# Kernel optimization log

Hardware: AMD Instinct MI355X
Metric: run time of the kernel (lower is better)

## Reference

```python
import jax, jax.numpy as jnp
import numpy as np
from jax import lax

B, T, C, H, N = 4, 1024, 2048, 32, 64
KVH = 8            # kv heads -> kv_dim = 512, n_rep = 4
GN_EPS = 0.00064   # group_norm eps from Step3


def _l2norm(x):
    # torch F.normalize(p=2, dim=-1) with eps=1e-12
    n = jnp.linalg.norm(x, axis=-1, keepdims=True)
    return x / jnp.maximum(n, 1e-12)


def _rwkv7_scan(r, decay, k, v, aa, bb, state):
    # all inputs (B,T,H,N); state (B,H,N,N) with layout [value, key]
    def step(S, inp):
        r_t, d_t, k_t, v_t, a_t, b_t = inp  # each (B,H,N)
        sa = jnp.einsum('bhik,bhk->bhi', S, a_t)
        S = (S * d_t[:, :, None, :]
             + sa[..., None] * b_t[:, :, None, :]
             + v_t[..., None] * k_t[:, :, None, :])
        y = jnp.einsum('bhik,bhk->bhi', S, r_t)
        return S, y
    xs = tuple(jnp.moveaxis(t, 1, 0) for t in (r, decay, k, v, aa, bb))  # (T,B,H,N)
    state, ys = lax.scan(step, state, xs)
    return jnp.moveaxis(ys, 0, 1), state  # (B,T,H,N), (B,H,N,N)


def _forward(x, v_first, state, R, R_bias, K, K_bias, V, V_bias, O, O_bias,
             w0, w1, w2, a0, a1, a2, v0, v1, v2, k_k, k_a, r_k, ln_w, ln_b):
    # ---- Step1: projections + gates (hybrid_matmul -> plain matmul in fp32 ref) ----
    r = x @ R.T + R_bias                                   # (B,T,C)
    w_raw = -jax.nn.softplus(-(w0 + jnp.tanh(x @ w1) @ w2)) - 0.6
    k = x @ K.T + K_bias                                   # (B,T,512)
    v = x @ V.T + V_bias
    n_rep = C // K.shape[0]
    k = jnp.repeat(k.reshape(B, T, KVH, N), n_rep, axis=2).reshape(B, T, C)
    v = jnp.repeat(v.reshape(B, T, KVH, N), n_rep, axis=2).reshape(B, T, C)
    a = jax.nn.sigmoid(a0 + (x @ a1) @ a2)
    kk = _l2norm((k * k_k).reshape(B, T, H, N)).reshape(B, T, C)
    k = k * (1.0 + (a - 1.0) * k_a)
    # layer_id != 0: cross-layer value blending
    v = v + (v_first - v) * jax.nn.sigmoid(v0 + (x @ v1) @ v2)
    aa = -kk
    bb = kk * a
    # ---- Step2: fused recurrent rwkv7 (fp32 state) ----
    decay = jnp.exp(-jnp.exp(w_raw.astype(jnp.float32)))
    rs = lambda t: t.astype(jnp.float32).reshape(B, T, H, N)
    y, state_out = _rwkv7_scan(rs(r), decay.reshape(B, T, H, N), rs(k), rs(v), rs(aa), rs(bb), state)
    # ---- Step3: group norm over (T, N) per (batch, head) as in the (B,C,T) permute ----
    mean = y.mean(axis=(1, 3), keepdims=True)
    var = ((y - mean) ** 2).mean(axis=(1, 3), keepdims=True)
    yn = (y - mean) * lax.rsqrt(var + GN_EPS)
    xx = (yn * ln_w.reshape(H, N) + ln_b.reshape(H, N)).reshape(B, T, C)
    bonus = ((r.reshape(B, T, H, N) * k.reshape(B, T, H, N) * r_k.reshape(H, N))
             .sum(-1, keepdims=True) * v.reshape(B, T, H, N)).reshape(B, T, C)
    xx = xx + bonus
    out = xx @ O.T + O_bias
    return out


def setup_inputs() -> dict:
    key = jax.random.key(0)
    ks = jax.random.split(key, 25)
    g = lambda i, shape, s: jax.random.normal(ks[i], shape, dtype=jnp.float32) * s
    return {
        'x': g(0, (B, T, C), 1.0),
        'v_first': g(1, (B, T, C), 1.0),
        'state': jnp.zeros((B, H, N, N), dtype=jnp.float32),
        'R': g(2, (C, C), 0.02), 'R_bias': jnp.zeros((C,), jnp.float32),
        'K': g(3, (KVH * N, C), 0.02), 'K_bias': jnp.zeros((KVH * N,), jnp.float32),
        'V': g(4, (KVH * N, C), 0.02), 'V_bias': jnp.zeros((KVH * N,), jnp.float32),
        'O': g(5, (C, C), 0.02), 'O_bias': jnp.zeros((C,), jnp.float32),
        'w0': g(6, (C,), 0.1), 'w1': g(7, (C, 64), 0.05), 'w2': g(8, (64, C), 0.05),
        'a0': g(9, (C,), 0.1), 'a1': g(10, (C, 64), 0.05), 'a2': g(11, (64, C), 0.05),
        'v0': g(12, (C,), 0.1), 'v1': g(13, (C, 32), 0.05), 'v2': g(14, (32, C), 0.05),
        'k_k': 1.0 + g(15, (C,), 0.05),
        'k_a': 1.0 + g(16, (C,), 0.05),
        'r_k': g(17, (C,), 0.1),
        'ln_w': jnp.ones((C,), jnp.float32),
        'ln_b': jnp.zeros((C,), jnp.float32),
    }


def reference(x, v_first, state, R, R_bias, K, K_bias, V, V_bias, O, O_bias,
              w0, w1, w2, a0, a1, a2, v0, v1, v2, k_k, k_a, r_k, ln_w, ln_b):
    return _forward(x, v_first, state, R, R_bias, K, K_bias, V, V_bias, O, O_bias,
                    w0, w1, w2, a0, a1, a2, v0, v1, v2, k_k, k_a, r_k, ln_w, ln_b)
```

## Files before the change

kernel.cpp:

```cpp
#include <hip/hip_runtime.h>
#include <hip/hip_bf16.h>
#include <math.h>

typedef __attribute__((ext_vector_type(8))) short bf16x8;
typedef __attribute__((ext_vector_type(4))) float f32x4;

__device__ __forceinline__ unsigned short f2b(float f) {
  unsigned u = __float_as_uint(f);
  unsigned r = (u + 0x7FFF + ((u >> 16) & 1)) >> 16;
  return (unsigned short)r;
}

__device__ __forceinline__ void async16(const void* g, void* l) {
  __builtin_amdgcn_global_load_lds(
      (const __attribute__((address_space(1))) unsigned int*)(g),
      (__attribute__((address_space(3))) unsigned int*)(l), 16, 0, 0);
}

__device__ __forceinline__ void async4(const void* g, void* l) {
  __builtin_amdgcn_global_load_lds(
      (const __attribute__((address_space(1))) unsigned int*)(g),
      (__attribute__((address_space(3))) unsigned int*)(l), 4, 0, 0);
}

__device__ __forceinline__ float rowsum16(float x) {
  x += __int_as_float(__builtin_amdgcn_update_dpp(0, __float_as_int(x), 0x121, 0xF, 0xF, false));
  x += __int_as_float(__builtin_amdgcn_update_dpp(0, __float_as_int(x), 0x122, 0xF, 0xF, false));
  x += __int_as_float(__builtin_amdgcn_update_dpp(0, __float_as_int(x), 0x124, 0xF, 0xF, false));
  x += __int_as_float(__builtin_amdgcn_update_dpp(0, __float_as_int(x), 0x128, 0xF, 0xF, false));
  return x;
}

__global__ __launch_bounds__(256) void cvt4_kernel(
    const float* __restrict__ x, const float* __restrict__ R,
    const float* __restrict__ K, const float* __restrict__ V,
    unsigned short* __restrict__ xb, unsigned short* __restrict__ RKVb)
{
  const int bid = blockIdx.x;
  const float* s; unsigned short* d; int i;
  if (bid < 8192)       { s = x; d = xb; i = bid * 256 + threadIdx.x; }
  else if (bid < 12288) { s = R; d = RKVb; i = (bid - 8192) * 256 + threadIdx.x; }
  else if (bid < 13312) { s = K; d = RKVb + 2048 * 2048; i = (bid - 12288) * 256 + threadIdx.x; }
  else                  { s = V; d = RKVb + 2560 * 2048; i = (bid - 13312) * 256 + threadIdx.x; }
  float4 v = ((const float4*)s)[i];
  ushort4 o;
  o.x = f2b(v.x); o.y = f2b(v.y); o.z = f2b(v.z); o.w = f2b(v.w);
  ((ushort4*)d)[i] = o;
}

__global__ __launch_bounds__(256) void cvt_bf16(
    const float* __restrict__ s, unsigned short* __restrict__ d, int n4)
{
  int i = blockIdx.x * 256 + threadIdx.x;
  if (i < n4) {
    float4 v = ((const float4*)s)[i];
    ushort4 o;
    o.x = f2b(v.x); o.y = f2b(v.y); o.z = f2b(v.z); o.w = f2b(v.w);
    ((ushort4*)d)[i] = o;
  }
}

__global__ __launch_bounds__(256) void tcvt_all(
    const float* __restrict__ w1, const float* __restrict__ a1,
    const float* __restrict__ v1, const float* __restrict__ w2,
    const float* __restrict__ a2, const float* __restrict__ v2,
    unsigned short* __restrict__ Bcat, unsigned short* __restrict__ w2t,
    unsigned short* __restrict__ a2t, unsigned short* __restrict__ v2t)
{
  const int r = blockIdx.x >> 5, i = blockIdx.x & 31;
  const float* in; unsigned short* out; int Kd, Nd, ors, bx, by;
  switch (r) {
    case 0:  in = w1; out = Bcat;             Kd = 2048; Nd = 64;   ors = 2048; bx = 0; by = i; break;
    case 1:  in = a1; out = Bcat + 64 * 2048; Kd = 2048; Nd = 64;   ors = 2048; bx = 0; by = i; break;
    case 2:  in = v1; out = Bcat + 128 * 2048; Kd = 2048; Nd = 32;  ors = 2048; bx = 0; by = i; break;
    case 3:  in = w2; out = w2t;              Kd = 64;   Nd = 2048; ors = 64;   bx = i; by = 0; break;
    case 4:  in = a2; out = a2t;              Kd = 64;   Nd = 2048; ors = 64;   bx = i; by = 0; break;
    default: in = v2; out = v2t;              Kd = 32;   Nd = 2048; ors = 32;   bx = i; by = 0; break;
  }
  __shared__ unsigned short tile[64][65];
  const int tx = threadIdx.x & 63, ty = threadIdx.x >> 6;
  const int n0 = bx * 64, k0 = by * 64;
  #pragma unroll
  for (int j = 0; j < 16; ++j) {
    const int k = k0 + j * 4 + ty;
    const int n = n0 + tx;
    unsigned short v = 0;
    if (k < Kd && n < Nd) v = f2b(in[(size_t)k * Nd + n]);
    tile[j * 4 + ty][tx] = v;
  }
  __syncthreads();
  #pragma unroll
  for (int j = 0; j < 16; ++j) {
    const int n = n0 + j * 4 + ty;
    const int k = k0 + tx;
    if (n < Nd && k < Kd) out[(size_t)n * ors + k] = tile[tx][j * 4 + ty];
  }
}

template<int OUTBF16, int ACT>
__global__ __launch_bounds__(256) void gemm_mfma(
    const unsigned short* __restrict__ A, int lda,
    const unsigned short* __restrict__ B, int ldb,
    const float* __restrict__ bias, void* __restrict__ Cv, int ldc,
    int M, int N, int K)
{
  __shared__ __align__(16) unsigned short As[128 * 32];
  __shared__ __align__(16) unsigned short Bs[128 * 32];
  const int tid = threadIdx.x;
  const int w = tid >> 6, lane = tid & 63;
  const int wr = (w >> 1) * 64, wc = (w & 1) * 64;
  const int row0 = blockIdx.y * 128, col0 = blockIdx.x * 128;

  f32x4 acc[4][4];
  #pragma unroll
  for (int i = 0; i < 4; ++i)
    #pragma unroll
    for (int j = 0; j < 4; ++j)
      acc[i][j] = (f32x4){0.f, 0.f, 0.f, 0.f};

  const int srow = w * 32 + (lane >> 2);
  const int scol = (lane & 3) * 8;
  const int brow0 = (col0 + srow < N) ? (col0 + srow) : 0;
  const int brow1 = (col0 + srow + 16 < N) ? (col0 + srow + 16) : 0;
  const unsigned short* gA0 = A + (size_t)(row0 + srow) * lda + scol;
  const unsigned short* gA1 = gA0 + (size_t)16 * lda;
  const unsigned short* gB0 = B + (size_t)brow0 * ldb + scol;
  const unsigned short* gB1 = B + (size_t)brow1 * ldb + scol;
  unsigned short* lA0 = As + w * 1024;
  unsigned short* lA1 = As + w * 1024 + 512;
  unsigned short* lB0 = Bs + w * 1024;
  unsigned short* lB1 = Bs + w * 1024 + 512;

  const int m16 = lane & 15;
  const int q8  = (lane >> 4) * 8;

  for (int k0 = 0; k0 < K; k0 += 32) {
    async16(gA0, lA0);
    async16(gA1, lA1);
    async16(gB0, lB0);
    async16(gB1, lB1);
    gA0 += 32; gA1 += 32; gB0 += 32; gB1 += 32;
    __syncthreads();
    bf16x8 af[4], bfr[4];
    #pragma unroll
    for (int i = 0; i < 4; ++i) {
      af[i]  = *(const bf16x8*)(As + (wr + i * 16 + m16) * 32 + q8);
      bfr[i] = *(const bf16x8*)(Bs + (wc + i * 16 + m16) * 32 + q8);
    }
    #pragma unroll
    for (int i = 0; i < 4; ++i)
      #pragma unroll
      for (int j = 0; j < 4; ++j)
        acc[i][j] = __builtin_amdgcn_mfma_f32_16x16x32_bf16(af[i], bfr[j], acc[i][j], 0, 0, 0);
    __syncthreads();
  }

  #pragma unroll
  for (int j = 0; j < 4; ++j) {
    const int c_ = col0 + wc + j * 16 + (lane & 15);
    if (c_ < N) {
      const float bv = bias ? bias[c_] : 0.f;
      #pragma unroll
      for (int i = 0; i < 4; ++i) {
        const int r_ = row0 + wr + i * 16 + (lane >> 4) * 4;
        #pragma unroll
        for (int t4 = 0; t4 < 4; ++t4) {
          float v = acc[i][j][t4] + bv;
          if (ACT == 2 && c_ < 64) v = tanhf(v);
          if (OUTBF16)
            ((unsigned short*)Cv)[(size_t)(r_ + t4) * ldc + c_] = f2b(v);
          else
            ((float*)Cv)[(size_t)(r_ + t4) * ldc + c_] = v;
        }
      }
    }
  }
}

__global__ __launch_bounds__(256) void gemm_rkv(
    const unsigned short* __restrict__ A, const unsigned short* __restrict__ B,
    const float* __restrict__ Rb_, const float* __restrict__ Kb_,
    const float* __restrict__ Vb_,
    float* __restrict__ Cr, float* __restrict__ Ck, float* __restrict__ Cvv)
{
  __shared__ __align__(16) unsigned short As[128 * 32];
  __shared__ __align__(16) unsigned short Bs[128 * 32];
  const int tid = threadIdx.x;
  const int w = tid >> 6, lane = tid & 63;
  const int wr = (w >> 1) * 64, wc = (w & 1) * 64;
  const int row0 = blockIdx.y * 128, col0 = blockIdx.x * 128;

  float* Cd; int ldc, cbase; const float* bias;
  if (col0 < 2048)      { Cd = Cr;  ldc = 2048; cbase = col0;        bias = Rb_; }
  else if (col0 < 2560) { Cd = Ck;  ldc = 512;  cbase = col0 - 2048; bias = Kb_; }
  else                  { Cd = Cvv; ldc = 512;  cbase = col0 - 2560; bias = Vb_; }

  f32x4 acc[4][4];
  #pragma unroll
  for (int i = 0; i < 4; ++i)
    #pragma unroll
    for (int j = 0; j < 4; ++j)
      acc[i][j] = (f32x4){0.f, 0.f, 0.f, 0.f};

  const int srow = w * 32 + (lane >> 2);
  const int scol = (lane & 3) * 8;
  const unsigned short* gA0 = A + (size_t)(row0 + srow) * 2048 + scol;
  const unsigned short* gA1 = gA0 + (size_t)16 * 2048;
  const unsigned short* gB0 = B + (size_t)(col0 + srow) * 2048 + scol;
  const unsigned short* gB1 = gB0 + (size_t)16 * 2048;
  unsigned short* lA0 = As + w * 1024;
  unsigned short* lA1 = As + w * 1024 + 512;
  unsigned short* lB0 = Bs + w * 1024;
  unsigned short* lB1 = Bs + w * 1024 + 512;

  const int m16 = lane & 15;
  const int q8  = (lane >> 4) * 8;

  for (int k0 = 0; k0 < 2048; k0 += 32) {
    async16(gA0, lA0);
    async16(gA1, lA1);
    async16(gB0, lB0);
    async16(gB1, lB1);
    gA0 += 32; gA1 += 32; gB0 += 32; gB1 += 32;
    __syncthreads();
    bf16x8 af[4], bfr[4];
    #pragma unroll
    for (int i = 0; i < 4; ++i) {
      af[i]  = *(const bf16x8*)(As + (wr + i * 16 + m16) * 32 + q8);
      bfr[i] = *(const bf16x8*)(Bs + (wc + i * 16 + m16) * 32 + q8);
    }
    #pragma unroll
    for (int i = 0; i < 4; ++i)
      #pragma unroll
      for (int j = 0; j < 4; ++j)
        acc[i][j] = __builtin_amdgcn_mfma_f32_16x16x32_bf16(af[i], bfr[j], acc[i][j], 0, 0, 0);
    __syncthreads();
  }

  #pragma unroll
  for (int j = 0; j < 4; ++j) {
    const int c_ = cbase + wc + j * 16 + (lane & 15);
    const float bv = bias[c_];
    #pragma unroll
    for (int i = 0; i < 4; ++i) {
      const int r_ = row0 + wr + i * 16 + (lane >> 4) * 4;
      #pragma unroll
      for (int t4 = 0; t4 < 4; ++t4)
        Cd[(size_t)(r_ + t4) * ldc + c_] = acc[i][j][t4] + bv;
    }
  }
}

__global__ __launch_bounds__(256) void prep_kernel(
    const float* __restrict__ k_buf, const float* __restrict__ v_buf,
    float* wt_decay, const float* __restrict__ at, float* vt_vf,
    const float* __restrict__ v_first,
    const float* __restrict__ w0, const float* __restrict__ a0,
    const float* __restrict__ v0, const float* __restrict__ k_k,
    const float* __restrict__ k_a,
    float* __restrict__ kf, float* __restrict__ aaq, float* __restrict__ bbq)
{
  const int row = blockIdx.x;
  const int tid = threadIdx.x;
  const int c0 = tid << 3;
  const int h = tid >> 3;
  const int kvoff = (h >> 2) << 6;
  const size_t base = (size_t)row * 2048;
  const size_t kvrow = (size_t)row * 512;
  float kr[8], kkr[8];
  float ss = 0.f;
  #pragma unroll
  for (int e = 0; e < 8; ++e) {
    const int c = c0 + e;
    const float kv = k_buf[kvrow + kvoff + (c & 63)];
    kr[e] = kv;
    const float t = kv * k_k[c];
    kkr[e] = t;
    ss = fmaf(t, t, ss);
  }
  ss += __shfl_xor(ss, 1);
  ss += __shfl_xor(ss, 2);
  ss += __shfl_xor(ss, 4);
  const float inv = 1.f / fmaxf(sqrtf(ss), 1e-12f);
  #pragma unroll
  for (int e = 0; e < 8; ++e) {
    const int c = c0 + e;
    const size_t idx = base + c;
    const float kk = kkr[e] * inv;
    const float a = 1.f / (1.f + expf(-(a0[c] + at[idx])));
    const float u = w0[c] + wt_decay[idx];
    const float sig_u = 1.f / (1.f + expf(-u));
    wt_decay[idx] = expf(-0.5488116360940264f * sig_u);
    kf[idx] = kr[e] * fmaf(a - 1.f, k_a[c], 1.f);
    const float vr = v_buf[kvrow + kvoff + (c & 63)];
    const float sv = 1.f / (1.f + expf(-(v0[c] + vt_vf[idx])));
    vt_vf[idx] = vr + (v_first[idx] - vr) * sv;
    aaq[idx] = -kk;
    bbq[idx] = kk * a;
  }
}

#define WB(n) asm volatile("s_waitcnt vmcnt(" #n ") lgkmcnt(0)\n\ts_barrier" ::: "memory")
#define BAR2() asm volatile("s_waitcnt lgkmcnt(0)\n\ts_barrier" ::: "memory")

__global__ __launch_bounds__(256) void scan_kernel(
    const float* __restrict__ rB, const float* __restrict__ dB,
    const float* __restrict__ kB, const float* __restrict__ vB,
    const float* __restrict__ aB, const float* __restrict__ bB,
    const float* __restrict__ state, float* __restrict__ y,
    float* __restrict__ part)
{
  __shared__ float lds[11776];
  const int tid = threadIdx.x;
  const int bid = blockIdx.x;
  const int xcd = bid & 7, j = bid >> 3;
  const int half = j & 1, bhq = j >> 1;
  const int bh = (bhq << 3) | xcd;
  const int widx = tid >> 6;
  const int lane = tid & 63;
  const int rg = lane >> 4;
  const int colg = lane & 15;
  const int r0b = (widx << 3) + (rg << 1);
  const int r0 = (half << 5) + r0b;
  const int b = bh >> 5, h = bh & 31;

  float4 S0 = *(const float4*)(state + (size_t)bh * 4096 + r0 * 64 + (colg << 2));
  float4 S1 = *(const float4*)(state + (size_t)bh * 4096 + (r0 + 1) * 64 + (colg << 2));

  const unsigned cb = (unsigned)((b * 1024) * 2048 + h * 64);
  const unsigned gcol = (unsigned)(colg << 2);
  const unsigned ldsseg = (unsigned)(widx << 8);
  const unsigned vrow = (unsigned)(half << 5);

  float sacc = 0.f, ssacc = 0.f;

  #define STAGE(step0, bofs) do {                                            \
    const unsigned go_ = cb + (unsigned)((step0) + (tid >> 4)) * 2048u;      \
    async16(rB + go_ + gcol, lds + (bofs) + 0 * 1024 + ldsseg);              \
    async16(dB + go_ + gcol, lds + (bofs) + 1 * 1024 + ldsseg);              \
    async16(kB + go_ + gcol, lds + (bofs) + 2 * 1024 + ldsseg);              \
    async16(aB + go_ + gcol, lds + (bofs) + 3 * 1024 + ldsseg);              \
    async16(bB + go_ + gcol, lds + (bofs) + 4 * 1024 + ldsseg);              \
    const unsigned gv0_ = cb + (unsigned)((step0) + (tid >> 5)) * 2048u      \
                          + vrow + (unsigned)(tid & 31);                     \
    async4(vB + gv0_, lds + (bofs) + 5120 + (widx << 6));                    \
    const unsigned t2_ = (unsigned)tid + 256u;                               \
    const unsigned gv1_ = cb + (unsigned)((step0) + (t2_ >> 5)) * 2048u      \
                          + vrow + (unsigned)(t2_ & 31);                     \
    async4(vB + gv1_, lds + (bofs) + 5120 + 256 + (widx << 6));              \
  } while (0)

  #define PROCESS(bofs) do {                                                 \
    const int orr_ = (bofs) + 0 * 1024 + (colg << 2);                        \
    const int od_  = (bofs) + 1 * 1024 + (colg << 2);                        \
    const int ok_  = (bofs) + 2 * 1024 + (colg << 2);                        \
    const int oa_  = (bofs) + 3 * 1024 + (colg << 2);                        \
    const int ob_  = (bofs) + 4 * 1024 + (colg << 2);                        \
    const int ov_  = (bofs) + 5120 + r0b;                                    \
    _Pragma("unroll")                                                        \
    for (int s = 0; s < 16; ++s) {                                           \
      const float4 av = *(const float4*)(lds + oa_ + s * 64);                \
      const float4 dv = *(const float4*)(lds + od_ + s * 64);                \
      const float4 bv = *(const float4*)(lds + ob_ + s * 64);                \
      const float4 kv = *(const float4*)(lds + ok_ + s * 64);                \
      const float4 rv = *(const float4*)(lds + orr_ + s * 64);               \
      const float2 vv = *(const float2*)(lds + ov_ + (s << 5));              \
      float t0a = fmaf(S0.y, av.y, S0.x * av.x);                             \
      t0a = fmaf(S0.z, av.z, t0a);                                           \
      t0a = fmaf(S0.w, av.w, t0a);                                           \
      float t0b = fmaf(S1.y, av.y, S1.x * av.x);                             \
      t0b = fmaf(S1.z, av.z, t0b);                                           \
      t0b = fmaf(S1.w, av.w, t0b);                                           \
      const float sa0 = rowsum16(t0a);                                       \
      const float sa1 = rowsum16(t0b);                                       \
      S0.x = fmaf(S0.x, dv.x, fmaf(sa0, bv.x, vv.x * kv.x));                 \
      S0.y = fmaf(S0.y, dv.y, fmaf(sa0, bv.y, vv.x * kv.y));                 \
      S0.z = fmaf(S0.z, dv.z, fmaf(sa0, bv.z, vv.x * kv.z));                 \
      S0.w = fmaf(S0.w, dv.w, fmaf(sa0, bv.w, vv.x * kv.w));                 \
      S1.x = fmaf(S1.x, dv.x, fmaf(sa1, bv.x, vv.y * kv.x));                 \
      S1.y = fmaf(S1.y, dv.y, fmaf(sa1, bv.y, vv.y * kv.y));                 \
      S1.z = fmaf(S1.z, dv.z, fmaf(sa1, bv.z, vv.y * kv.z));                 \
      S1.w = fmaf(S1.w, dv.w, fmaf(sa1, bv.w, vv.y * kv.w));                 \
      float t1a = fmaf(S0.y, rv.y, S0.x * rv.x);                             \
      t1a = fmaf(S0.z, rv.z, t1a);                                           \
      t1a = fmaf(S0.w, rv.w, t1a);                                           \
      float t1b = fmaf(S1.y, rv.y, S1.x * rv.x);                             \
      t1b = fmaf(S1.z, rv.z, t1b);                                           \
      t1b = fmaf(S1.w, rv.w, t1b);                                           \
      const float y0 = rowsum16(t1a);                                        \
      const float y1 = rowsum16(t1b);                                        \
      if (colg == 0) {                                                       \
        *(float2*)(lds + 11264 + (s << 5) + r0b) = make_float2(y0, y1);      \
        sacc += y0 + y1;                                                     \
        ssacc = fmaf(y0, y0, fmaf(y1, y1, ssacc));                           \
      }                                                                      \
    }                                                                        \
  } while (0)

  #define YSTORE(step0) do {                                                 \
    const float2 v_ = *(const float2*)(lds + 11264 + ((tid >> 4) << 5)       \
                                       + ((tid & 15) << 1));                 \
    *(float2*)(y + cb + (unsigned)((step0) + (tid >> 4)) * 2048u             \
               + vrow + (unsigned)((tid & 15) << 1)) = v_;                   \
  } while (0)

  STAGE(0, 0);
  STAGE(16, 5632);

  WB(7);
  PROCESS(0);
  BAR2();
  YSTORE(0);
  STAGE(32, 0);

  for (int c = 1; c <= 62; ++c) {
    const int bofs = (c & 1) ? 5632 : 0;
    WB(8);
    PROCESS(bofs);
    BAR2();
    YSTORE(c << 4);
    if (c < 62) STAGE((c + 2) << 4, bofs);
  }

  WB(1);
  PROCESS(5632);
  BAR2();
  YSTORE(1008);

  sacc  += __shfl_xor(sacc, 16);
  sacc  += __shfl_xor(sacc, 32);
  ssacc += __shfl_xor(ssacc, 16);
  ssacc += __shfl_xor(ssacc, 32);
  __syncthreads();
  if (lane == 0) { lds[widx] = sacc; lds[4 + widx] = ssacc; }
  __syncthreads();
  if (tid == 0) {
    const float s_  = lds[0] + lds[1] + lds[2] + lds[3];
    const float ss_ = lds[4] + lds[5] + lds[6] + lds[7];
    ((float2*)part)[(bh << 1) + half] = make_float2(s_, ss_);
  }

  #undef STAGE
  #undef PROCESS
  #undef YSTORE
}

__global__ __launch_bounds__(256) void gapply_kernel(
    const float* __restrict__ y, const float* __restrict__ rB,
    const float* __restrict__ kf, const float* __restrict__ vf,
    const float* __restrict__ part, const float* __restrict__ r_k,
    const float* __restrict__ ln_w, const float* __restrict__ ln_b,
    unsigned short* __restrict__ xxb)
{
  const int row = blockIdx.x;
  const int b = row >> 10;
  const int tid = threadIdx.x;
  const int h = tid >> 3;
  const int bh = b * 32 + h;
  float s = 0.f, ss = 0.f;
  #pragma unroll
  for (int j = 0; j < 2; ++j) {
    const float2 pr = ((const float2*)part)[(bh << 1) + j];
    s += pr.x; ss += pr.y;
  }
  const float mean = s * (1.f / 65536.f);
  const float rstd = rsqrtf(ss * (1.f / 65536.f) - mean * mean + 0.00064f);
  const int c0 = tid << 3;
  const size_t base = (size_t)row * 2048 + c0;
  float yv[8], vv[8];
  float p = 0.f;
  #pragma unroll
  for (int e = 0; e < 8; ++e) {
    yv[e] = y[base + e];
    vv[e] = vf[base + e];
    p = fmaf(rB[base + e] * kf[base + e], r_k[c0 + e], p);
  }
  p += __shfl_xor(p, 1);
  p += __shfl_xor(p, 2);
  p += __shfl_xor(p, 4);
  #pragma unroll
  for (int e = 0; e < 8; ++e) {
    const float yn = (yv[e] - mean) * rstd;
    xxb[base + e] = f2b(fmaf(yn, ln_w[c0 + e], ln_b[c0 + e]) + p * vv[e]);
  }
}

extern "C" void kernel_launch(void* const* d_in, const int* in_sizes, int n_in,
                              void* d_out, int out_size, void* d_ws, size_t ws_size,
                              hipStream_t stream) {
  const float* x       = (const float*)d_in[0];
  const float* v_first = (const float*)d_in[1];
  const float* state   = (const float*)d_in[2];
  const float* Rw      = (const float*)d_in[3];
  const float* R_bias  = (const float*)d_in[4];
  const float* Kw      = (const float*)d_in[5];
  const float* K_bias  = (const float*)d_in[6];
  const float* Vw      = (const float*)d_in[7];
  const float* V_bias  = (const float*)d_in[8];
  const float* Ow      = (const float*)d_in[9];
  const float* O_bias  = (const float*)d_in[10];
  const float* w0      = (const float*)d_in[11];
  const float* w1      = (const float*)d_in[12];
  const float* w2      = (const float*)d_in[13];
  const float* a0      = (const float*)d_in[14];
  const float* a1      = (const float*)d_in[15];
  const float* a2      = (const float*)d_in[16];
  const float* v0      = (const float*)d_in[17];
  const float* v1      = (const float*)d_in[18];
  const float* v2      = (const float*)d_in[19];
  const float* k_k     = (const float*)d_in[20];
  const float* k_a     = (const float*)d_in[21];
  const float* r_k     = (const float*)d_in[22];
  const float* ln_w    = (const float*)d_in[23];
  const float* ln_b    = (const float*)d_in[24];

  float* ws = (float*)d_ws;
  float* r_buf = ws;
  float* k_buf = r_buf + 8388608;
  float* v_buf = k_buf + 2097152;
  float* wt    = v_buf + 2097152;
  float* at    = wt    + 8388608;
  float* vt    = at    + 8388608;
  float* kf    = vt    + 8388608;
  float* aaq   = kf    + 8388608;
  float* bbq   = aaq   + 8388608;
  float* part  = bbq   + 8388608;
  unsigned short* xb   = (unsigned short*)bbq;
  unsigned short* RKVb = (unsigned short*)kf;
  unsigned short* hcat = (unsigned short*)(kf + 3200000);
  unsigned short* Bcat = (unsigned short*)(kf + 3600000);
  unsigned short* w2t  = (unsigned short*)(kf + 3800000);
  unsigned short* a2t  = (unsigned short*)(kf + 3900000);
  unsigned short* v2t  = (unsigned short*)(kf + 4000000);
  unsigned short* Ob   = (unsigned short*)wt;
  unsigned short* xxb  = (unsigned short*)aaq;

  dim3 blk(256);
  cvt4_kernel<<<14336, blk, 0, stream>>>(x, Rw, Kw, Vw, xb, RKVb);
  tcvt_all<<<192, blk, 0, stream>>>(w1, a1, v1, w2, a2, v2, Bcat, w2t, a2t, v2t);
  gemm_mfma<1,2><<<dim3(2, 32), blk, 0, stream>>>(xb, 2048, Bcat, 2048, nullptr,
                                                  hcat, 160, 4096, 160, 2048);
  gemm_rkv<<<dim3(24, 32), blk, 0, stream>>>(xb, RKVb, R_bias, K_bias, V_bias,
                                             r_buf, k_buf, v_buf);
  gemm_mfma<0,0><<<dim3(16, 32), blk, 0, stream>>>(hcat, 160, w2t, 64, nullptr,
                                                   wt, 2048, 4096, 2048, 64);
  gemm_mfma<0,0><<<dim3(16, 32), blk, 0, stream>>>(hcat + 64, 160, a2t, 64, nullptr,
                                                   at, 2048, 4096, 2048, 64);
  gemm_mfma<0,0><<<dim3(16, 32), blk, 0, stream>>>(hcat + 128, 160, v2t, 32, nullptr,
                                                   vt, 2048, 4096, 2048, 32);
  prep_kernel<<<4096, blk, 0, stream>>>(k_buf, v_buf, wt, at, vt, v_first,
                                        w0, a0, v0, k_k, k_a, kf, aaq, bbq);
  float* ybuf = at;
  scan_kernel<<<256, blk, 0, stream>>>(r_buf, wt, kf, vt, aaq, bbq, state, ybuf,
                                       part);
  cvt_bf16<<<4096, blk, 0, stream>>>(Ow, Ob, 1048576);
  gapply_kernel<<<4096, blk, 0, stream>>>(ybuf, r_buf, kf, vt, part, r_k,
                                          ln_w, ln_b, xxb);
  gemm_mfma<0,0><<<dim3(16, 32), blk, 0, stream>>>(xxb, 2048, Ob, 2048, O_bias,
                                                   (float*)d_out, 2048, 4096, 2048, 2048);
}
```

Before: 823.2 us.

## Pack r/k and a/b as bf16 pairs and split scan over 4 row blocks

```diff
diff --git a/kernel.cpp b/kernel.cpp
--- a/kernel.cpp
+++ b/kernel.cpp
@@ -15,12 +15,6 @@
   __builtin_amdgcn_global_load_lds(
       (const __attribute__((address_space(1))) unsigned int*)(g),
       (__attribute__((address_space(3))) unsigned int*)(l), 16, 0, 0);
-}
-
-__device__ __forceinline__ void async4(const void* g, void* l) {
-  __builtin_amdgcn_global_load_lds(
-      (const __attribute__((address_space(1))) unsigned int*)(g),
-      (__attribute__((address_space(3))) unsigned int*)(l), 4, 0, 0);
 }
 
 __device__ __forceinline__ float rowsum16(float x) {
@@ -253,12 +247,13 @@
 
 __global__ __launch_bounds__(256) void prep_kernel(
     const float* __restrict__ k_buf, const float* __restrict__ v_buf,
+    const float* __restrict__ r_buf,
     float* wt_decay, const float* __restrict__ at, float* vt_vf,
     const float* __restrict__ v_first,
     const float* __restrict__ w0, const float* __restrict__ a0,
     const float* __restrict__ v0, const float* __restrict__ k_k,
     const float* __restrict__ k_a,
-    float* __restrict__ kf, float* __restrict__ aaq, float* __restrict__ bbq)
+    unsigned* __restrict__ rk_pk, unsigned* __restrict__ ab_pk)
 {
   const int row = blockIdx.x;
   const int tid = threadIdx.x;
@@ -291,12 +286,12 @@
     const float u = w0[c] + wt_decay[idx];
     const float sig_u = 1.f / (1.f + expf(-u));
     wt_decay[idx] = expf(-0.5488116360940264f * sig_u);
-    kf[idx] = kr[e] * fmaf(a - 1.f, k_a[c], 1.f);
+    const float kfin = kr[e] * fmaf(a - 1.f, k_a[c], 1.f);
     const float vr = v_buf[kvrow + kvoff + (c & 63)];
     const float sv = 1.f / (1.f + expf(-(v0[c] + vt_vf[idx])));
     vt_vf[idx] = vr + (v_first[idx] - vr) * sv;
-    aaq[idx] = -kk;
-    bbq[idx] = kk * a;
+    rk_pk[idx] = ((unsigned)f2b(kfin) << 16) | (unsigned)f2b(r_buf[idx]);
+    ab_pk[idx] = ((unsigned)f2b(-kk) << 16) | (unsigned)f2b(kk * a);
   }
 }
 
@@ -304,128 +299,119 @@
 #define BAR2() asm volatile("s_waitcnt lgkmcnt(0)\n\ts_barrier" ::: "memory")
 
 __global__ __launch_bounds__(256) void scan_kernel(
-    const float* __restrict__ rB, const float* __restrict__ dB,
-    const float* __restrict__ kB, const float* __restrict__ vB,
-    const float* __restrict__ aB, const float* __restrict__ bB,
+    const unsigned* __restrict__ rkB, const unsigned* __restrict__ abB,
+    const float* __restrict__ dB, const float* __restrict__ vB,
     const float* __restrict__ state, float* __restrict__ y,
     float* __restrict__ part)
 {
-  __shared__ float lds[11776];
+  __shared__ float lds[6912];
+  unsigned* ldsU = (unsigned*)lds;
   const int tid = threadIdx.x;
   const int bid = blockIdx.x;
-  const int xcd = bid & 7, j = bid >> 3;
-  const int half = j & 1, bhq = j >> 1;
-  const int bh = (bhq << 3) | xcd;
+  const int xcd = bid & 7, bj = bid >> 3;
+  const int m = bj & 3, gq = bj >> 2;
+  const int bh = (gq << 3) | xcd;
   const int widx = tid >> 6;
   const int lane = tid & 63;
   const int rg = lane >> 4;
   const int colg = lane & 15;
-  const int r0b = (widx << 3) + (rg << 1);
-  const int r0 = (half << 5) + r0b;
+  const int rowb = (widx << 2) + rg;
+  const int row = (m << 4) + rowb;
   const int b = bh >> 5, h = bh & 31;
 
-  float4 S0 = *(const float4*)(state + (size_t)bh * 4096 + r0 * 64 + (colg << 2));
-  float4 S1 = *(const float4*)(state + (size_t)bh * 4096 + (r0 + 1) * 64 + (colg << 2));
+  float4 S = *(const float4*)(state + (size_t)bh * 4096 + row * 64 + (colg << 2));
 
   const unsigned cb = (unsigned)((b * 1024) * 2048 + h * 64);
-  const unsigned gcol = (unsigned)(colg << 2);
-  const unsigned ldsseg = (unsigned)(widx << 8);
-  const unsigned vrow = (unsigned)(half << 5);
+  const unsigned sstep = (unsigned)(tid >> 4);
+  const unsigned scol = (unsigned)((tid & 15) << 2);
+  const unsigned lseg = (unsigned)(widx << 8);
 
   float sacc = 0.f, ssacc = 0.f;
 
   #define STAGE(step0, bofs) do {                                            \
-    const unsigned go_ = cb + (unsigned)((step0) + (tid >> 4)) * 2048u;      \
-    async16(rB + go_ + gcol, lds + (bofs) + 0 * 1024 + ldsseg);              \
-    async16(dB + go_ + gcol, lds + (bofs) + 1 * 1024 + ldsseg);              \
-    async16(kB + go_ + gcol, lds + (bofs) + 2 * 1024 + ldsseg);              \
-    async16(aB + go_ + gcol, lds + (bofs) + 3 * 1024 + ldsseg);              \
-    async16(bB + go_ + gcol, lds + (bofs) + 4 * 1024 + ldsseg);              \
-    const unsigned gv0_ = cb + (unsigned)((step0) + (tid >> 5)) * 2048u      \
-                          + vrow + (unsigned)(tid & 31);                     \
-    async4(vB + gv0_, lds + (bofs) + 5120 + (widx << 6));                    \
-    const unsigned t2_ = (unsigned)tid + 256u;                               \
-    const unsigned gv1_ = cb + (unsigned)((step0) + (t2_ >> 5)) * 2048u      \
-                          + vrow + (unsigned)(t2_ & 31);                     \
-    async4(vB + gv1_, lds + (bofs) + 5120 + 256 + (widx << 6));              \
+    const unsigned go_ = cb + ((step0) + sstep) * 2048u + scol;              \
+    async16(rkB + go_, ldsU + (bofs) + lseg);                                \
+    async16(abB + go_, ldsU + (bofs) + 1024 + lseg);                         \
+    async16(dB + go_,  lds + (bofs) + 2048 + lseg);                          \
+    if (lane < 16) {                                                         \
+      const unsigned gv_ = cb + ((step0) + (unsigned)(widx << 2)             \
+                                 + (unsigned)(lane >> 2)) * 2048u            \
+                           + (unsigned)(m << 4) + (unsigned)((lane & 3) << 2); \
+      async16(vB + gv_, lds + (bofs) + 3072 + (widx << 6));                  \
+    }                                                                        \
   } while (0)
 
   #define PROCESS(bofs) do {                                                 \
-    const int orr_ = (bofs) + 0 * 1024 + (colg << 2);                        \
-    const int od_  = (bofs) + 1 * 1024 + (colg << 2);                        \
-    const int ok_  = (bofs) + 2 * 1024 + (colg << 2);                        \
-    const int oa_  = (bofs) + 3 * 1024 + (colg << 2);                        \
-    const int ob_  = (bofs) + 4 * 1024 + (colg << 2);                        \
-    const int ov_  = (bofs) + 5120 + r0b;                                    \
     _Pragma("unroll")                                                        \
     for (int s = 0; s < 16; ++s) {                                           \
-      const float4 av = *(const float4*)(lds + oa_ + s * 64);                \
-      const float4 dv = *(const float4*)(lds + od_ + s * 64);                \
-      const float4 bv = *(const float4*)(lds + ob_ + s * 64);                \
-      const float4 kv = *(const float4*)(lds + ok_ + s * 64);                \
-      const float4 rv = *(const float4*)(lds + orr_ + s * 64);               \
-      const float2 vv = *(const float2*)(lds + ov_ + (s << 5));              \
-      float t0a = fmaf(S0.y, av.y, S0.x * av.x);                             \
-      t0a = fmaf(S0.z, av.z, t0a);                                           \
-      t0a = fmaf(S0.w, av.w, t0a);                                           \
-      float t0b = fmaf(S1.y, av.y, S1.x * av.x);                             \
-      t0b = fmaf(S1.z, av.z, t0b);                                           \
-      t0b = fmaf(S1.w, av.w, t0b);                                           \
-      const float sa0 = rowsum16(t0a);                                       \
-      const float sa1 = rowsum16(t0b);                                       \
-      S0.x = fmaf(S0.x, dv.x, fmaf(sa0, bv.x, vv.x * kv.x));                 \
-      S0.y = fmaf(S0.y, dv.y, fmaf(sa0, bv.y, vv.x * kv.y));                 \
-      S0.z = fmaf(S0.z, dv.z, fmaf(sa0, bv.z, vv.x * kv.z));                 \
-      S0.w = fmaf(S0.w, dv.w, fmaf(sa0, bv.w, vv.x * kv.w));                 \
-      S1.x = fmaf(S1.x, dv.x, fmaf(sa1, bv.x, vv.y * kv.x));                 \
-      S1.y = fmaf(S1.y, dv.y, fmaf(sa1, bv.y, vv.y * kv.y));                 \
-      S1.z = fmaf(S1.z, dv.z, fmaf(sa1, bv.z, vv.y * kv.z));                 \
-      S1.w = fmaf(S1.w, dv.w, fmaf(sa1, bv.w, vv.y * kv.w));                 \
-      float t1a = fmaf(S0.y, rv.y, S0.x * rv.x);                             \
-      t1a = fmaf(S0.z, rv.z, t1a);                                           \
-      t1a = fmaf(S0.w, rv.w, t1a);                                           \
-      float t1b = fmaf(S1.y, rv.y, S1.x * rv.x);                             \
-      t1b = fmaf(S1.z, rv.z, t1b);                                           \
-      t1b = fmaf(S1.w, rv.w, t1b);                                           \
-      const float y0 = rowsum16(t1a);                                        \
-      const float y1 = rowsum16(t1b);                                        \
+      const uint4 rkw = *(const uint4*)(ldsU + (bofs) + s * 64 + (colg << 2)); \
+      const uint4 abw = *(const uint4*)(ldsU + (bofs) + 1024 + s * 64 + (colg << 2)); \
+      const float4 dv = *(const float4*)(lds + (bofs) + 2048 + s * 64 + (colg << 2)); \
+      const float vv = lds[(bofs) + 3072 + (s << 4) + rowb];                 \
+      const float aa0 = __uint_as_float(abw.x & 0xffff0000u);                \
+      const float aa1 = __uint_as_float(abw.y & 0xffff0000u);                \
+      const float aa2 = __uint_as_float(abw.z & 0xffff0000u);                \
+      const float aa3 = __uint_as_float(abw.w & 0xffff0000u);                \
+      const float bb0 = __uint_as_float(abw.x << 16);                        \
+      const float bb1 = __uint_as_float(abw.y << 16);                        \
+      const float bb2 = __uint_as_float(abw.z << 16);                        \
+      const float bb3 = __uint_as_float(abw.w << 16);                        \
+      const float k0 = __uint_as_float(rkw.x & 0xffff0000u);                 \
+      const float k1 = __uint_as_float(rkw.y & 0xffff0000u);                 \
+      const float k2 = __uint_as_float(rkw.z & 0xffff0000u);                 \
+      const float k3 = __uint_as_float(rkw.w & 0xffff0000u);                 \
+      const float r0 = __uint_as_float(rkw.x << 16);                         \
+      const float r1 = __uint_as_float(rkw.y << 16);                         \
+      const float r2 = __uint_as_float(rkw.z << 16);                         \
+      const float r3 = __uint_as_float(rkw.w << 16);                         \
+      float t0 = fmaf(S.y, aa1, S.x * aa0);                                  \
+      t0 = fmaf(S.z, aa2, t0);                                               \
+      t0 = fmaf(S.w, aa3, t0);                                               \
+      const float sa = rowsum16(t0);                                         \
+      S.x = fmaf(S.x, dv.x, fmaf(sa, bb0, vv * k0));                         \
+      S.y = fmaf(S.y, dv.y, fmaf(sa, bb1, vv * k1));                         \
+      S.z = fmaf(S.z, dv.z, fmaf(sa, bb2, vv * k2));                         \
+      S.w = fmaf(S.w, dv.w, fmaf(sa, bb3, vv * k3));                         \
+      float t1 = fmaf(S.y, r1, S.x * r0);                                    \
+      t1 = fmaf(S.z, r2, t1);                                                \
+      t1 = fmaf(S.w, r3, t1);                                                \
+      const float yv = rowsum16(t1);                                         \
       if (colg == 0) {                                                       \
-        *(float2*)(lds + 11264 + (s << 5) + r0b) = make_float2(y0, y1);      \
-        sacc += y0 + y1;                                                     \
-        ssacc = fmaf(y0, y0, fmaf(y1, y1, ssacc));                           \
+        lds[6656 + (s << 4) + rowb] = yv;                                    \
+        sacc += yv;                                                          \
+        ssacc = fmaf(yv, yv, ssacc);                                         \
       }                                                                      \
     }                                                                        \
   } while (0)
 
   #define YSTORE(step0) do {                                                 \
-    const float2 v_ = *(const float2*)(lds + 11264 + ((tid >> 4) << 5)       \
-                                       + ((tid & 15) << 1));                 \
-    *(float2*)(y + cb + (unsigned)((step0) + (tid >> 4)) * 2048u             \
-               + vrow + (unsigned)((tid & 15) << 1)) = v_;                   \
+    const float val_ = lds[6656 + tid];                                      \
+    y[cb + ((step0) + (unsigned)(tid >> 4)) * 2048u +                        \
+      (unsigned)(m << 4) + (unsigned)(tid & 15)] = val_;                     \
   } while (0)
 
-  STAGE(0, 0);
-  STAGE(16, 5632);
-
-  WB(7);
+  STAGE(0u, 0);
+  STAGE(16u, 3328);
+
+  WB(4);
   PROCESS(0);
   BAR2();
-  YSTORE(0);
-  STAGE(32, 0);
+  YSTORE(0u);
+  STAGE(32u, 0);
 
   for (int c = 1; c <= 62; ++c) {
-    const int bofs = (c & 1) ? 5632 : 0;
-    WB(8);
+    const int bofs = (c & 1) ? 3328 : 0;
+    WB(5);
     PROCESS(bofs);
     BAR2();
-    YSTORE(c << 4);
-    if (c < 62) STAGE((c + 2) << 4, bofs);
+    YSTORE((unsigned)(c << 4));
+    if (c < 62) STAGE((unsigned)((c + 2) << 4), bofs);
   }
 
   WB(1);
-  PROCESS(5632);
+  PROCESS(3328);
   BAR2();
-  YSTORE(1008);
+  YSTORE(1008u);
 
   sacc  += __shfl_xor(sacc, 16);
   sacc  += __shfl_xor(sacc, 32);
@@ -437,7 +423,7 @@
   if (tid == 0) {
     const float s_  = lds[0] + lds[1] + lds[2] + lds[3];
     const float ss_ = lds[4] + lds[5] + lds[6] + lds[7];
-    ((float2*)part)[(bh << 1) + half] = make_float2(s_, ss_);
+    ((float2*)part)[(bh << 2) + m] = make_float2(s_, ss_);
   }
 
   #undef STAGE
@@ -446,8 +432,8 @@
 }
 
 __global__ __launch_bounds__(256) void gapply_kernel(
-    const float* __restrict__ y, const float* __restrict__ rB,
-    const float* __restrict__ kf, const float* __restrict__ vf,
+    const float* __restrict__ y, const unsigned* __restrict__ rkB,
+    const float* __restrict__ vf,
     const float* __restrict__ part, const float* __restrict__ r_k,
     const float* __restrict__ ln_w, const float* __restrict__ ln_b,
     unsigned short* __restrict__ xxb)
@@ -459,8 +445,8 @@
   const int bh = b * 32 + h;
   float s = 0.f, ss = 0.f;
   #pragma unroll
-  for (int j = 0; j < 2; ++j) {
-    const float2 pr = ((const float2*)part)[(bh << 1) + j];
+  for (int j = 0; j < 4; ++j) {
+    const float2 pr = ((const float2*)part)[(bh << 2) + j];
     s += pr.x; ss += pr.y;
   }
   const float mean = s * (1.f / 65536.f);
@@ -473,7 +459,10 @@
   for (int e = 0; e < 8; ++e) {
     yv[e] = y[base + e];
     vv[e] = vf[base + e];
-    p = fmaf(rB[base + e] * kf[base + e], r_k[c0 + e], p);
+    const unsigned w_ = rkB[base + e];
+    const float rr = __uint_as_float(w_ << 16);
+    const float kk_ = __uint_as_float(w_ & 0xffff0000u);
+    p = fmaf(rr * kk_, r_k[c0 + e], p);
   }
   p += __shfl_xor(p, 1);
   p += __shfl_xor(p, 2);
@@ -532,8 +521,10 @@
   unsigned short* w2t  = (unsigned short*)(kf + 3800000);
   unsigned short* a2t  = (unsigned short*)(kf + 3900000);
   unsigned short* v2t  = (unsigned short*)(kf + 4000000);
+  unsigned* rk_pk      = (unsigned*)aaq;
+  unsigned* ab_pk      = (unsigned*)bbq;
   unsigned short* Ob   = (unsigned short*)wt;
-  unsigned short* xxb  = (unsigned short*)aaq;
+  unsigned short* xxb  = (unsigned short*)bbq;
 
   dim3 blk(256);
   cvt4_kernel<<<14336, blk, 0, stream>>>(x, Rw, Kw, Vw, xb, RKVb);
@@ -548,13 +539,12 @@
                                                    at, 2048, 4096, 2048, 64);
   gemm_mfma<0,0><<<dim3(16, 32), blk, 0, stream>>>(hcat + 128, 160, v2t, 32, nullptr,
                                                    vt, 2048, 4096, 2048, 32);
-  prep_kernel<<<4096, blk, 0, stream>>>(k_buf, v_buf, wt, at, vt, v_first,
-                                        w0, a0, v0, k_k, k_a, kf, aaq, bbq);
+  prep_kernel<<<4096, blk, 0, stream>>>(k_buf, v_buf, r_buf, wt, at, vt, v_first,
+                                        w0, a0, v0, k_k, k_a, rk_pk, ab_pk);
   float* ybuf = at;
-  scan_kernel<<<256, blk, 0, stream>>>(r_buf, wt, kf, vt, aaq, bbq, state, ybuf,
-                                       part);
+  scan_kernel<<<512, blk, 0, stream>>>(rk_pk, ab_pk, wt, vt, state, ybuf, part);
   cvt_bf16<<<4096, blk, 0, stream>>>(Ow, Ob, 1048576);
-  gapply_kernel<<<4096, blk, 0, stream>>>(ybuf, r_buf, kf, vt, part, r_k,
+  gapply_kernel<<<4096, blk, 0, stream>>>(ybuf, rk_pk, vt, part, r_k,
                                           ln_w, ln_b, xxb);
   gemm_mfma<0,0><<<dim3(16, 32), blk, 0, stream>>>(xxb, 2048, Ob, 2048, O_bias,
                                                    (float*)d_out, 2048, 4096, 2048, 2048);
```

Measured after the change: 765.6 us. -7.0%, faster.
